# Kernel optimization log

Hardware: AMD Instinct MI355X
Metric: run time of the kernel (lower is better)

The kernel has to match this reference:

```python
import jax, jax.numpy as jnp
import numpy as np

N_NODES = 50000
N_EDGES = 800000
D_IN, H1, H2, N_CLASSES = 128, 128, 64, 2


def setup_inputs() -> dict:
    key = jax.random.key(0)
    ks = jax.random.split(key, 8)
    x = jax.random.normal(ks[0], (N_NODES, D_IN), dtype=jnp.float32)
    edge_index = jax.random.randint(ks[1], (2, N_EDGES), 0, N_NODES, dtype=jnp.int64)
    s = 1.0 / np.sqrt(D_IN)
    W1 = jax.random.uniform(ks[2], (D_IN, H1), jnp.float32, -s, s)
    b1 = jnp.zeros((H1,), jnp.float32)
    s = 1.0 / np.sqrt(H1)
    W2 = jax.random.uniform(ks[3], (H1, H2), jnp.float32, -s, s)
    b2 = jnp.zeros((H2,), jnp.float32)
    s = 1.0 / np.sqrt(H2)
    Wo = jax.random.uniform(ks[4], (H2, N_CLASSES), jnp.float32, -s, s)
    bo = jax.random.uniform(ks[5], (N_CLASSES,), jnp.float32, -s, s)
    return {"x": x, "edge_index": edge_index, "W1": W1, "b1": b1,
            "W2": W2, "b2": b2, "Wo": Wo, "bo": bo}


def _gcn_conv(x, W, b, src, dst, n_nodes):
    # PyG GCNConv: add self loops, symmetric normalization deg^{-1/2} A deg^{-1/2}
    h = x @ W  # [N, out]
    ones = jnp.ones((src.shape[0],), h.dtype)
    deg = jax.ops.segment_sum(ones, dst, num_segments=n_nodes) + 1.0  # +1 self loop
    dinv = jax.lax.rsqrt(deg)  # deg >= 1 always (self loops)
    coef = dinv[src] * dinv[dst]  # [E]
    msg = h[src] * coef[:, None]  # [E, out] gather
    agg = jax.ops.segment_sum(msg, dst, num_segments=n_nodes)  # scatter-add
    agg = agg + h * (dinv * dinv)[:, None]  # self-loop contribution
    return agg + b


def reference(x, edge_index, W1, b1, W2, b2, Wo, bo):
    src, dst = edge_index[0], edge_index[1]
    n = x.shape[0]
    h = jax.nn.relu(_gcn_conv(x, W1, b1, src, dst, n))
    # dropout p=0.25 is identity in eval mode
    h = jax.nn.relu(_gcn_conv(h, W2, b2, src, dst, n))
    logits = h @ Wo + bo
    return jax.nn.log_softmax(logits, axis=1)
```

## Files before the change

### kernel.cpp

```cpp
#include <hip/hip_runtime.h>
#include <stdint.h>

#define N_NODES 50000
#define N_EDGES 800000
#define CAP 80
#define ZROW N_NODES
#define NBIN 196
#define NBLK_A 128
#define EPB 6250
#define GEMM_BLOCKS 782

typedef __attribute__((ext_vector_type(8))) short short8;
typedef __attribute__((ext_vector_type(4))) float floatx4;

__device__ __forceinline__ float bflo(uint32_t u) { return __uint_as_float(u << 16); }
__device__ __forceinline__ float bfhi(uint32_t u) { return __uint_as_float(u & 0xffff0000u); }
__device__ __forceinline__ unsigned short f2b(float f) {
    uint32_t u = __float_as_uint(f);
    u += 0x7fffu + ((u >> 16) & 1u);
    return (unsigned short)(u >> 16);
}

__global__ __launch_bounds__(256) void k_prep(const float* __restrict__ W1,
                                              const float* __restrict__ W2,
                                              unsigned short* __restrict__ Wt1,
                                              unsigned short* __restrict__ Wt2,
                                              const int* __restrict__ dst,
                                              int* __restrict__ mat) {
    __shared__ int h[NBIN];
    int t = threadIdx.x, blk = blockIdx.x;
    if (blk < NBLK_A) {
        if (t < NBIN) h[t] = 0;
        __syncthreads();
        int e0 = blk * EPB;
        for (int i = t; i < EPB; i += 256) atomicAdd(&h[dst[e0 + i] >> 8], 1);
        __syncthreads();
        if (t < NBIN) mat[blk * NBIN + t] = h[t];
        return;
    }
    int gid = (blk - NBLK_A) * 256 + t;
    if (gid < 16384) {
        int k = gid >> 7, n = gid & 127;
        Wt1[n * 128 + k] = f2b(W1[gid]);
    } else if (gid < 24576) {
        int j = gid - 16384;
        int k = j >> 6, n = j & 63;
        Wt2[n * 128 + k] = f2b(W2[j]);
    }
}

__global__ __launch_bounds__(256) void k_scan(int* __restrict__ mat,
                                              int* __restrict__ binStart) {
    __shared__ int tot[256];
    int b = threadIdx.x;
    int base = 0;
    if (b < NBIN) {
        #pragma unroll 8
        for (int k = 0; k < NBLK_A; k++) {
            int v = mat[k * NBIN + b];
            mat[k * NBIN + b] = base;
            base += v;
        }
    }
    tot[b] = (b < NBIN) ? base : 0;
    __syncthreads();
    if (b == 0) {
        int r = 0;
        for (int i = 0; i < NBIN; i++) { int v = tot[i]; tot[i] = r; r += v; }
    }
    __syncthreads();
    if (b < NBIN) {
        int bb = tot[b];
        binStart[b] = bb;
        #pragma unroll 8
        for (int k = 0; k < NBLK_A; k++) mat[k * NBIN + b] += bb;
        if (b == NBIN - 1) binStart[NBIN] = bb + base;
    }
}

__global__ __launch_bounds__(256) void k_binscat(const int* __restrict__ src,
                                                 const int* __restrict__ dst,
                                                 const int* __restrict__ mat,
                                                 int2* __restrict__ binned) {
    __shared__ int cur[NBIN];
    int t = threadIdx.x, blk = blockIdx.x;
    if (t < NBIN) cur[t] = mat[blk * NBIN + t];
    __syncthreads();
    int e0 = blk * EPB;
    for (int i = t; i < EPB; i += 256) {
        int d = dst[e0 + i], s = src[e0 + i];
        int slot = atomicAdd(&cur[d >> 8], 1);
        binned[slot] = make_int2(s, d);
    }
}

__global__ __launch_bounds__(256) void k_csr_gemm1(const int2* __restrict__ binned,
                                                   const int* __restrict__ binStart,
                                                   int* __restrict__ counts,
                                                   int* __restrict__ csr,
                                                   const float* __restrict__ x,
                                                   const unsigned short* __restrict__ Wt1,
                                                   unsigned short* __restrict__ h1s,
                                                   unsigned short* __restrict__ h2s) {
    __shared__ unsigned short At[64 * 136];
    __shared__ unsigned short Bt[128 * 136];
    __shared__ int cnt[256];
    int t = threadIdx.x;
    if (blockIdx.x < NBIN) {
        cnt[t] = 0;
        __syncthreads();
        int b = blockIdx.x;
        int st = binStart[b], en = binStart[b + 1];
        for (int i = st + t; i < en; i += 256) {
            int2 e = binned[i];
            int r = atomicAdd(&cnt[e.y & 255], 1);
            if (r < CAP) csr[e.y * CAP + r] = e.x;
        }
        __syncthreads();
        counts[b * 256 + t] = cnt[t];
        return;
    }
    int row0 = (blockIdx.x - NBIN) * 64;
    for (int i = t; i < 2048; i += 256) {
        int n = i >> 4, kc = (i & 15) * 8;
        *(uint4*)&Bt[n * 136 + kc] = *(const uint4*)(Wt1 + n * 128 + kc);
    }
    for (int i = t; i < 1024; i += 256) {
        int r = i >> 4, kc = (i & 15) * 8;
        int g = row0 + r; if (g >= N_NODES) g = N_NODES - 1;
        const float* p = x + g * 128 + kc;
        float4 a = *(const float4*)p, b = *(const float4*)(p + 4);
        uint4 o;
        o.x = (uint32_t)f2b(a.x) | ((uint32_t)f2b(a.y) << 16);
        o.y = (uint32_t)f2b(a.z) | ((uint32_t)f2b(a.w) << 16);
        o.z = (uint32_t)f2b(b.x) | ((uint32_t)f2b(b.y) << 16);
        o.w = (uint32_t)f2b(b.z) | ((uint32_t)f2b(b.w) << 16);
        *(uint4*)&At[r * 136 + kc] = o;
    }
    __syncthreads();
    int wv = t >> 6, lane = t & 63;
    int m = lane & 15, qd = lane >> 4;
    floatx4 acc[8];
    #pragma unroll
    for (int c = 0; c < 8; c++) acc[c] = (floatx4){0.f, 0.f, 0.f, 0.f};
    const unsigned short* ap = &At[(wv * 16 + m) * 136 + qd * 8];
    const unsigned short* bp = &Bt[m * 136 + qd * 8];
    #pragma unroll
    for (int kk = 0; kk < 4; kk++) {
        short8 af = *(const short8*)(ap + kk * 32);
        #pragma unroll
        for (int c = 0; c < 8; c++) {
            short8 bf = *(const short8*)(bp + c * 16 * 136 + kk * 32);
            acc[c] = __builtin_amdgcn_mfma_f32_16x16x32_bf16(af, bf, acc[c], 0, 0, 0);
        }
    }
    #pragma unroll
    for (int reg = 0; reg < 4; reg++) {
        int g = row0 + wv * 16 + qd * 4 + reg;
        if (g < N_NODES) {
            #pragma unroll
            for (int c = 0; c < 8; c++)
                h1s[g * 128 + c * 16 + m] = f2b(acc[c][reg]);
        } else {
            #pragma unroll
            for (int c = 0; c < 8; c++)
                h1s[g * 128 + c * 16 + m] = 0;
            #pragma unroll
            for (int c = 0; c < 4; c++)
                h2s[g * 64 + c * 16 + m] = 0;
        }
    }
}

__global__ __launch_bounds__(256) void k_agg1g2(const unsigned short* __restrict__ h1s,
                                                const unsigned short* __restrict__ Wt2,
                                                const int* __restrict__ csr,
                                                const int* __restrict__ counts,
                                                const float* __restrict__ b1,
                                                unsigned short* __restrict__ h2s) {
    __shared__ unsigned short Bt[64 * 136];
    __shared__ unsigned short At[16 * 136];
    int t = threadIdx.x;
    for (int i = t; i < 1024; i += 256) {
        int n = i >> 4, kc = (i & 15) * 8;
        *(uint4*)&Bt[n * 136 + kc] = *(const uint4*)(Wt2 + n * 128 + kc);
    }
    int wv = t >> 6, lane = t & 63;
    int q = lane >> 4, l = lane & 15;
    int v0 = blockIdx.x * 16;
    int v = v0 + wv * 4 + q;
    int n = counts[v];
    float dv = rsqrtf((float)n + 1.0f);
    int n_eff = min(n, CAP);
    const int* cs = csr + v * CAP;
    int nmax = n_eff;
    nmax = max(nmax, __shfl_xor(nmax, 16));
    nmax = max(nmax, __shfl_xor(nmax, 32));
    float a0, a1, a2, a3, a4, a5, a6, a7;
    {
        uint4 p = *(const uint4*)(h1s + v * 128 + l * 8);
        a0 = dv * bflo(p.x); a1 = dv * bfhi(p.x); a2 = dv * bflo(p.y); a3 = dv * bfhi(p.y);
        a4 = dv * bflo(p.z); a5 = dv * bfhi(p.z); a6 = dv * bflo(p.w); a7 = dv * bfhi(p.w);
    }
    for (int base = 0; base < nmax; base += 16) {
        int idx = base + l;
        int e = (idx < n_eff) ? cs[idx] : ZROW;
        float de = rsqrtf((float)counts[e] + 1.0f);
        int mm = nmax - base; if (mm > 16) mm = 16;
        #pragma unroll 4
        for (int i = 0; i < mm; i++) {
            int s = __shfl(e, (q << 4) + i);
            float di = __shfl(de, (q << 4) + i);
            uint4 p = *(const uint4*)(h1s + s * 128 + l * 8);
            a0 = fmaf(di, bflo(p.x), a0); a1 = fmaf(di, bfhi(p.x), a1);
            a2 = fmaf(di, bflo(p.y), a2); a3 = fmaf(di, bfhi(p.y), a3);
            a4 = fmaf(di, bflo(p.z), a4); a5 = fmaf(di, bfhi(p.z), a5);
            a6 = fmaf(di, bflo(p.w), a6); a7 = fmaf(di, bfhi(p.w), a7);
        }
    }
    {
        float4 bL = *(const float4*)(b1 + l * 8);
        float4 bH = *(const float4*)(b1 + l * 8 + 4);
        a0 = fmaxf(fmaf(dv, a0, bL.x), 0.f); a1 = fmaxf(fmaf(dv, a1, bL.y), 0.f);
        a2 = fmaxf(fmaf(dv, a2, bL.z), 0.f); a3 = fmaxf(fmaf(dv, a3, bL.w), 0.f);
        a4 = fmaxf(fmaf(dv, a4, bH.x), 0.f); a5 = fmaxf(fmaf(dv, a5, bH.y), 0.f);
        a6 = fmaxf(fmaf(dv, a6, bH.z), 0.f); a7 = fmaxf(fmaf(dv, a7, bH.w), 0.f);
        uint4 o;
        o.x = (uint32_t)f2b(a0) | ((uint32_t)f2b(a1) << 16);
        o.y = (uint32_t)f2b(a2) | ((uint32_t)f2b(a3) << 16);
        o.z = (uint32_t)f2b(a4) | ((uint32_t)f2b(a5) << 16);
        o.w = (uint32_t)f2b(a6) | ((uint32_t)f2b(a7) << 16);
        *(uint4*)&At[(wv * 4 + q) * 136 + l * 8] = o;
    }
    __syncthreads();
    int m = lane & 15, qd = lane >> 4;
    floatx4 acc = (floatx4){0.f, 0.f, 0.f, 0.f};
    const unsigned short* ap = &At[m * 136 + qd * 8];
    const unsigned short* bp = &Bt[(wv * 16 + m) * 136 + qd * 8];
    #pragma unroll
    for (int kk = 0; kk < 4; kk++) {
        short8 af = *(const short8*)(ap + kk * 32);
        short8 bf = *(const short8*)(bp + kk * 32);
        acc = __builtin_amdgcn_mfma_f32_16x16x32_bf16(af, bf, acc, 0, 0, 0);
    }
    #pragma unroll
    for (int reg = 0; reg < 4; reg++) {
        int g = v0 + qd * 4 + reg;
        float dg = rsqrtf((float)counts[g] + 1.0f);
        h2s[g * 64 + wv * 16 + m] = f2b(dg * acc[reg]);
    }
}

__global__ __launch_bounds__(256) void k_agg2(const unsigned short* __restrict__ h2s,
                                              const int* __restrict__ csr,
                                              const int* __restrict__ counts,
                                              const float* __restrict__ b2,
                                              const float* __restrict__ Wo,
                                              const float* __restrict__ bo,
                                              float* __restrict__ out) {
    int wave = (blockIdx.x * 256 + threadIdx.x) >> 6;
    int lane = threadIdx.x & 63;
    int q = lane >> 4, l = lane & 15;
    int h = l >> 3, c = l & 7;
    int v = wave * 4 + q;
    int n = counts[v];
    float dv = rsqrtf((float)n + 1.0f);
    int n_eff = min(n, CAP);
    const int* cs = csr + v * CAP;
    int nmax = n_eff;
    nmax = max(nmax, __shfl_xor(nmax, 16));
    nmax = max(nmax, __shfl_xor(nmax, 32));
    float a0 = 0.f, a1 = 0.f, a2 = 0.f, a3 = 0.f, a4 = 0.f, a5 = 0.f, a6 = 0.f, a7 = 0.f;
    if (h == 0) {
        uint4 p = *(const uint4*)(h2s + v * 64 + c * 8);
        a0 = bflo(p.x); a1 = bfhi(p.x); a2 = bflo(p.y); a3 = bfhi(p.y);
        a4 = bflo(p.z); a5 = bfhi(p.z); a6 = bflo(p.w); a7 = bfhi(p.w);
    }
    for (int base = 0; base < nmax; base += 16) {
        int idx = base + l;
        int e = (idx < n_eff) ? cs[idx] : ZROW;
        int mm = nmax - base; if (mm > 16) mm = 16;
        int pairs = (mm + 1) >> 1;
        #pragma unroll 4
        for (int i = 0; i < pairs; i++) {
            int s = __shfl(e, (q << 4) + 2 * i + h);
            uint4 p = *(const uint4*)(h2s + s * 64 + c * 8);
            a0 += bflo(p.x); a1 += bfhi(p.x); a2 += bflo(p.y); a3 += bfhi(p.y);
            a4 += bflo(p.z); a5 += bfhi(p.z); a6 += bflo(p.w); a7 += bfhi(p.w);
        }
    }
    a0 += __shfl_xor(a0, 8); a1 += __shfl_xor(a1, 8);
    a2 += __shfl_xor(a2, 8); a3 += __shfl_xor(a3, 8);
    a4 += __shfl_xor(a4, 8); a5 += __shfl_xor(a5, 8);
    a6 += __shfl_xor(a6, 8); a7 += __shfl_xor(a7, 8);
    float4 bL = *(const float4*)(b2 + c * 8);
    float4 bH = *(const float4*)(b2 + c * 8 + 4);
    a0 = fmaxf(fmaf(dv, a0, bL.x), 0.f); a1 = fmaxf(fmaf(dv, a1, bL.y), 0.f);
    a2 = fmaxf(fmaf(dv, a2, bL.z), 0.f); a3 = fmaxf(fmaf(dv, a3, bL.w), 0.f);
    a4 = fmaxf(fmaf(dv, a4, bH.x), 0.f); a5 = fmaxf(fmaf(dv, a5, bH.y), 0.f);
    a6 = fmaxf(fmaf(dv, a6, bH.z), 0.f); a7 = fmaxf(fmaf(dv, a7, bH.w), 0.f);
    float4 wA = *(const float4*)(Wo + c * 16);
    float4 wB = *(const float4*)(Wo + c * 16 + 4);
    float4 wC = *(const float4*)(Wo + c * 16 + 8);
    float4 wD = *(const float4*)(Wo + c * 16 + 12);
    float l0 = a0 * wA.x + a1 * wA.z + a2 * wB.x + a3 * wB.z
             + a4 * wC.x + a5 * wC.z + a6 * wD.x + a7 * wD.z;
    float l1 = a0 * wA.y + a1 * wA.w + a2 * wB.y + a3 * wB.w
             + a4 * wC.y + a5 * wC.w + a6 * wD.y + a7 * wD.w;
    l0 += __shfl_xor(l0, 1); l1 += __shfl_xor(l1, 1);
    l0 += __shfl_xor(l0, 2); l1 += __shfl_xor(l1, 2);
    l0 += __shfl_xor(l0, 4); l1 += __shfl_xor(l1, 4);
    if (l == 0) {
        float2 bof = *(const float2*)bo;
        l0 += bof.x; l1 += bof.y;
        float m = fmaxf(l0, l1);
        float ls = m + __logf(__expf(l0 - m) + __expf(l1 - m));
        *(float2*)(out + v * 2) = make_float2(l0 - ls, l1 - ls);
    }
}

extern "C" void kernel_launch(void* const* d_in, const int* in_sizes, int n_in,
                              void* d_out, int out_size, void* d_ws, size_t ws_size,
                              hipStream_t stream) {
    const float* x  = (const float*)d_in[0];
    const int* ei   = (const int*)d_in[1];
    const float* W1 = (const float*)d_in[2];
    const float* b1 = (const float*)d_in[3];
    const float* W2 = (const float*)d_in[4];
    const float* b2 = (const float*)d_in[5];
    const float* Wo = (const float*)d_in[6];
    const float* bo = (const float*)d_in[7];
    float* out      = (float*)d_out;
    const int* src = ei;
    const int* dst = ei + N_EDGES;

    char* w = (char*)d_ws;
    int* counts = (int*)(w + 0);
    int* csr    = (int*)(w + 200704);
    unsigned short* Wt1 = (unsigned short*)(w + 16200704);
    unsigned short* Wt2 = (unsigned short*)(w + 16233472);
    unsigned short* h1s = (unsigned short*)(w + 16249856);
    unsigned short* h2s = (unsigned short*)(w + 29062144);
    int2* binned = (int2*)(w + 35468288);
    int* mat     = (int*)(w + 41868288);
    int* binStart= (int*)(w + 41968640);

    k_prep     <<<224, 256, 0, stream>>>(W1, W2, Wt1, Wt2, dst, mat);
    k_scan     <<<1, 256, 0, stream>>>(mat, binStart);
    k_binscat  <<<NBLK_A, 256, 0, stream>>>(src, dst, mat, binned);
    k_csr_gemm1<<<NBIN + GEMM_BLOCKS, 256, 0, stream>>>(binned, binStart, counts, csr,
                                                        x, Wt1, h1s, h2s);
    k_agg1g2   <<<3125, 256, 0, stream>>>(h1s, Wt2, csr, counts, b1, h2s);
    k_agg2     <<<3125, 256, 0, stream>>>(h2s, csr, counts, b2, Wo, bo, out);
}
```

Baseline: 185.7 us.

## Fuse edge binning scatter with GEMM1 and pack binned edges to 32 bits

Moves the edge bin-scatter work into the same launch as the first GEMM, so the scatter blocks run alongside the GEMM blocks. CSR construction becomes its own small kernel that runs afterwards. Binned edges are packed as a 16-bit source plus an 8-bit local destination in one uint32, which halves that traffic; this relies on node ids fitting in 16 bits, but N=50000 is below 65536, so it holds. The histogram matrix is transposed so the scan reads contiguous columns. The launch count stays the same, and the GEMM now overlaps with the scatter instead of with CSR building.

```diff
diff --git a/kernel.cpp b/kernel.cpp
--- a/kernel.cpp
+++ b/kernel.cpp
@@ -35,7 +35,7 @@
         int e0 = blk * EPB;
         for (int i = t; i < EPB; i += 256) atomicAdd(&h[dst[e0 + i] >> 8], 1);
         __syncthreads();
-        if (t < NBIN) mat[blk * NBIN + t] = h[t];
+        if (t < NBIN) mat[t * NBLK_A + blk] = h[t];
         return;
     }
     int gid = (blk - NBLK_A) * 256 + t;
@@ -55,72 +55,52 @@
     int b = threadIdx.x;
     int base = 0;
     if (b < NBIN) {
+        int* col = mat + b * NBLK_A;
         #pragma unroll 8
-        for (int k = 0; k < NBLK_A; k++) {
-            int v = mat[k * NBIN + b];
-            mat[k * NBIN + b] = base;
-            base += v;
-        }
+        for (int k = 0; k < NBLK_A; k++) { int v = col[k]; col[k] = base; base += v; }
     }
     tot[b] = (b < NBIN) ? base : 0;
     __syncthreads();
     if (b == 0) {
         int r = 0;
         for (int i = 0; i < NBIN; i++) { int v = tot[i]; tot[i] = r; r += v; }
+        binStart[NBIN] = r;
     }
     __syncthreads();
     if (b < NBIN) {
         int bb = tot[b];
         binStart[b] = bb;
+        int* col = mat + b * NBLK_A;
         #pragma unroll 8
-        for (int k = 0; k < NBLK_A; k++) mat[k * NBIN + b] += bb;
-        if (b == NBIN - 1) binStart[NBIN] = bb + base;
-    }
-}
-
-__global__ __launch_bounds__(256) void k_binscat(const int* __restrict__ src,
-                                                 const int* __restrict__ dst,
-                                                 const int* __restrict__ mat,
-                                                 int2* __restrict__ binned) {
-    __shared__ int cur[NBIN];
-    int t = threadIdx.x, blk = blockIdx.x;
-    if (t < NBIN) cur[t] = mat[blk * NBIN + t];
-    __syncthreads();
-    int e0 = blk * EPB;
-    for (int i = t; i < EPB; i += 256) {
-        int d = dst[e0 + i], s = src[e0 + i];
-        int slot = atomicAdd(&cur[d >> 8], 1);
-        binned[slot] = make_int2(s, d);
-    }
-}
-
-__global__ __launch_bounds__(256) void k_csr_gemm1(const int2* __restrict__ binned,
-                                                   const int* __restrict__ binStart,
-                                                   int* __restrict__ counts,
-                                                   int* __restrict__ csr,
-                                                   const float* __restrict__ x,
-                                                   const unsigned short* __restrict__ Wt1,
-                                                   unsigned short* __restrict__ h1s,
-                                                   unsigned short* __restrict__ h2s) {
+        for (int k = 0; k < NBLK_A; k++) col[k] += bb;
+    }
+}
+
+__global__ __launch_bounds__(256) void k_binscat_gemm1(const int* __restrict__ src,
+                                                       const int* __restrict__ dst,
+                                                       const int* __restrict__ mat,
+                                                       uint32_t* __restrict__ binned,
+                                                       const float* __restrict__ x,
+                                                       const unsigned short* __restrict__ Wt1,
+                                                       unsigned short* __restrict__ h1s,
+                                                       unsigned short* __restrict__ h2s) {
     __shared__ unsigned short At[64 * 136];
     __shared__ unsigned short Bt[128 * 136];
-    __shared__ int cnt[256];
     int t = threadIdx.x;
-    if (blockIdx.x < NBIN) {
-        cnt[t] = 0;
+    if (blockIdx.x < NBLK_A) {
+        int* cur = (int*)At;
+        int blk = blockIdx.x;
+        if (t < NBIN) cur[t] = mat[t * NBLK_A + blk];
         __syncthreads();
-        int b = blockIdx.x;
-        int st = binStart[b], en = binStart[b + 1];
-        for (int i = st + t; i < en; i += 256) {
-            int2 e = binned[i];
-            int r = atomicAdd(&cnt[e.y & 255], 1);
-            if (r < CAP) csr[e.y * CAP + r] = e.x;
-        }
-        __syncthreads();
-        counts[b * 256 + t] = cnt[t];
+        int e0 = blk * EPB;
+        for (int i = t; i < EPB; i += 256) {
+            int d = dst[e0 + i], s = src[e0 + i];
+            int slot = atomicAdd(&cur[d >> 8], 1);
+            binned[slot] = (uint32_t)s | ((uint32_t)(d & 255) << 16);
+        }
         return;
     }
-    int row0 = (blockIdx.x - NBIN) * 64;
+    int row0 = (blockIdx.x - NBLK_A) * 64;
     for (int i = t; i < 2048; i += 256) {
         int n = i >> 4, kc = (i & 15) * 8;
         *(uint4*)&Bt[n * 136 + kc] = *(const uint4*)(Wt1 + n * 128 + kc);
@@ -170,6 +150,26 @@
                 h2s[g * 64 + c * 16 + m] = 0;
         }
     }
+}
+
+__global__ __launch_bounds__(256) void k_csr(const uint32_t* __restrict__ binned,
+                                             const int* __restrict__ binStart,
+                                             int* __restrict__ counts,
+                                             int* __restrict__ csr) {
+    __shared__ int cnt[256];
+    int t = threadIdx.x, b = blockIdx.x;
+    cnt[t] = 0;
+    __syncthreads();
+    int st = binStart[b], en = binStart[b + 1];
+    int node0 = b << 8;
+    for (int i = st + t; i < en; i += 256) {
+        uint32_t w = binned[i];
+        int doff = (int)(w >> 16);
+        int r = atomicAdd(&cnt[doff], 1);
+        if (r < CAP) csr[(node0 + doff) * CAP + r] = (int)(w & 0xffffu);
+    }
+    __syncthreads();
+    counts[node0 + t] = cnt[t];
 }
 
 __global__ __launch_bounds__(256) void k_agg1g2(const unsigned short* __restrict__ h1s,
@@ -341,15 +341,15 @@
     unsigned short* Wt2 = (unsigned short*)(w + 16233472);
     unsigned short* h1s = (unsigned short*)(w + 16249856);
     unsigned short* h2s = (unsigned short*)(w + 29062144);
-    int2* binned = (int2*)(w + 35468288);
-    int* mat     = (int*)(w + 41868288);
-    int* binStart= (int*)(w + 41968640);
-
-    k_prep     <<<224, 256, 0, stream>>>(W1, W2, Wt1, Wt2, dst, mat);
-    k_scan     <<<1, 256, 0, stream>>>(mat, binStart);
-    k_binscat  <<<NBLK_A, 256, 0, stream>>>(src, dst, mat, binned);
-    k_csr_gemm1<<<NBIN + GEMM_BLOCKS, 256, 0, stream>>>(binned, binStart, counts, csr,
-                                                        x, Wt1, h1s, h2s);
-    k_agg1g2   <<<3125, 256, 0, stream>>>(h1s, Wt2, csr, counts, b1, h2s);
-    k_agg2     <<<3125, 256, 0, stream>>>(h2s, csr, counts, b2, Wo, bo, out);
-}
+    uint32_t* binned = (uint32_t*)(w + 35468288);
+    int* mat     = (int*)(w + 38668288);
+    int* binStart= (int*)(w + 38768640);
+
+    k_prep         <<<224, 256, 0, stream>>>(W1, W2, Wt1, Wt2, dst, mat);
+    k_scan         <<<1, 256, 0, stream>>>(mat, binStart);
+    k_binscat_gemm1<<<NBLK_A + GEMM_BLOCKS, 256, 0, stream>>>(src, dst, mat, binned,
+                                                              x, Wt1, h1s, h2s);
+    k_csr          <<<NBIN, 256, 0, stream>>>(binned, binStart, counts, csr);
+    k_agg1g2       <<<3125, 256, 0, stream>>>(h1s, Wt2, csr, counts, b1, h2s);
+    k_agg2         <<<3125, 256, 0, stream>>>(h2s, csr, counts, b2, Wo, bo, out);
+}
```

New measurement: 186.5 us. Within noise of the previous version (+0.4%).
